# Optimization experiments

Hardware: AMD Instinct MI355X
Metric: run time of the kernel (lower is better)

## Reference

```python
import jax, jax.numpy as jnp
import numpy as np

D_MODEL, D_CTX, D_HEAD = 1024, 768, 16

def setup_inputs() -> dict:
    key = jax.random.key(0)
    ks = jax.random.split(key, 10)
    B, M, N = 8, 4096, 4096
    s = lambda d: 1.0 / np.sqrt(d)
    return {
        "x": jax.random.normal(ks[0], (B, M, D_MODEL), dtype=jnp.float32),
        "context": jax.random.normal(ks[1], (B, N, D_CTX), dtype=jnp.float32),
        "Wq": jax.random.uniform(ks[2], (D_MODEL, D_HEAD), jnp.float32, -s(D_MODEL), s(D_MODEL)),
        "bq": jax.random.uniform(ks[3], (D_HEAD,), jnp.float32, -s(D_MODEL), s(D_MODEL)),
        "Wk": jax.random.uniform(ks[4], (D_CTX, D_HEAD), jnp.float32, -s(D_CTX), s(D_CTX)),
        "bk": jax.random.uniform(ks[5], (D_HEAD,), jnp.float32, -s(D_CTX), s(D_CTX)),
        "Wv": jax.random.uniform(ks[6], (D_CTX, D_HEAD), jnp.float32, -s(D_CTX), s(D_CTX)),
        "bv": jax.random.uniform(ks[7], (D_HEAD,), jnp.float32, -s(D_CTX), s(D_CTX)),
        "Wo": jax.random.uniform(ks[8], (D_HEAD, D_MODEL), jnp.float32, -s(D_HEAD), s(D_HEAD)),
        "bo": jax.random.uniform(ks[9], (D_MODEL,), jnp.float32, -s(D_HEAD), s(D_HEAD)),
    }

def _kernel(t):
    # ELU+1 feature map (non-negative)
    return jax.nn.elu(t) + 1.0

def reference(x, context, Wq, bq, Wk, bk, Wv, bv, Wo, bo):
    Q = _kernel(x @ Wq + bq)            # (B, M, d_head)
    K = _kernel(context @ Wk + bk)      # (B, N, d_head)
    V = context @ Wv + bv               # (B, N, d_head)
    KtV = jnp.einsum('bnd,bne->bde', K, V)   # (B, d_head, d_head)
    num = jnp.einsum('bmd,bde->bme', Q, KtV) # (B, M, d_head)
    K_sum = K.sum(axis=1)                    # (B, d_head)
    denom = jnp.einsum('bmd,bd->bm', Q, K_sum)[..., None] + 1e-6
    out = num / denom                        # (B, M, d_head)
    return out @ Wo + bo                     # (B, M, d_model)
```

## Files before the change

### kernel.cpp

```cpp
#include <hip/hip_runtime.h>
#include <math.h>

#define B_   8
#define M_   4096
#define N_   4096
#define DM   1024
#define DC   768
#define DH   16
#define CHUNKS 64
#define PD   8

typedef float v4f __attribute__((ext_vector_type(4)));
typedef __attribute__((ext_vector_type(8))) short short8v;
typedef __attribute__((ext_vector_type(4))) float f32x4;
typedef __attribute__((ext_vector_type(4))) int int4v;

__device__ __forceinline__ float elu1(float t) {
    return t > 0.0f ? t + 1.0f : expf(t);
}
__device__ __forceinline__ float4 ld4(const float* p) { return *reinterpret_cast<const float4*>(p); }
__device__ __forceinline__ void  st4(float* p, float4 v) { *reinterpret_cast<float4*>(p) = v; }
__device__ __forceinline__ void  st4nt(float* p, float4 v) {
    v4f w; w.x = v.x; w.y = v.y; w.z = v.z; w.w = v.w;
    __builtin_nontemporal_store(w, reinterpret_cast<v4f*>(p));
}
__device__ __forceinline__ void fma4(float4& a, float s, float4 w) {
    a.x = fmaf(s, w.x, a.x); a.y = fmaf(s, w.y, a.y);
    a.z = fmaf(s, w.z, a.z); a.w = fmaf(s, w.w, a.w);
}
__device__ __forceinline__ short f2bf(float f) {
    unsigned u = __float_as_uint(f);
    unsigned r = 0x7FFFu + ((u >> 16) & 1u);
    return (short)((u + r) >> 16);
}
__device__ __forceinline__ unsigned cvtpk(float a, float b) {
    unsigned r;
    asm("v_cvt_pk_bf16_f32 %0, %1, %2" : "=v"(r) : "v"(a), "v"(b));
    return r;
}
__device__ __forceinline__ short8v mk_frag(const float4& a, const float4& b) {
    int4v iv;
    iv.x = (int)cvtpk(a.x, a.y);
    iv.y = (int)cvtpk(a.z, a.w);
    iv.z = (int)cvtpk(b.x, b.y);
    iv.w = (int)cvtpk(b.z, b.w);
    union { int4v i; short8v s; } u; u.i = iv;
    return u.s;
}

__global__ __launch_bounds__(256) void prep(
    const float* __restrict__ Wq, const float* __restrict__ Wk,
    const float* __restrict__ Wv,
    short* __restrict__ fq, short* __restrict__ fk, short* __restrict__ fv)
{
    const int id = blockIdx.x * 256 + threadIdx.x;
    if (id >= 80 * 64) return;
    const int l  = id & 63;
    const int kt = id >> 6;
    const float* W; short* dst; int ktl;
    if (kt < 32)      { W = Wq; dst = fq; ktl = kt; }
    else if (kt < 56) { W = Wk; dst = fk; ktl = kt - 32; }
    else              { W = Wv; dst = fv; ktl = kt - 56; }
    const int k0 = ktl * 32 + (l >> 4) * 8;
    const int d  = l & 15;
    short* o = dst + ((size_t)ktl * 64 + l) * 8;
    #pragma unroll
    for (int j = 0; j < 8; ++j)
        o[j] = f2bf(W[(size_t)(k0 + j) * DH + d]);
}

__global__ __launch_bounds__(256) void fused1(
    const float* __restrict__ ctx, const float* __restrict__ x,
    const short* __restrict__ fq, const short* __restrict__ fk,
    const short* __restrict__ fv,
    const float* __restrict__ bq, const float* __restrict__ bk,
    const float* __restrict__ bv,
    float* __restrict__ part, float* __restrict__ q_ws)
{
    __shared__ float sk[64][DH+1];
    __shared__ float sv[64][DH+1];

    const int t  = threadIdx.x;
    const int l  = t & 63;
    const int w  = t >> 6;
    const int g4 = l >> 4;
    const int lr = l & 15;

    float4 pa[PD], pb[PD];

    if (blockIdx.x < B_*N_/64) {
        const size_t row0 = (size_t)blockIdx.x * 64;
        const float* src = ctx + (row0 + w*16 + lr) * DC + g4*8;
        f32x4 accK = {0,0,0,0}, accV = {0,0,0,0};

        #pragma unroll
        for (int i = 0; i < PD; ++i) {
            pa[i] = ld4(src + i*32);
            pb[i] = ld4(src + i*32 + 4);
        }
        #pragma unroll
        for (int kt = 0; kt < 24; ++kt) {
            const int st = kt & (PD-1);
            const short8v a = mk_frag(pa[st], pb[st]);
            if (kt + PD < 24) {
                pa[st] = ld4(src + (kt+PD)*32);
                pb[st] = ld4(src + (kt+PD)*32 + 4);
            }
            const short8v bkf = *reinterpret_cast<const short8v*>(fk + ((size_t)kt*64 + l)*8);
            const short8v bvf = *reinterpret_cast<const short8v*>(fv + ((size_t)kt*64 + l)*8);
            accK = __builtin_amdgcn_mfma_f32_16x16x32_bf16(a, bkf, accK, 0, 0, 0);
            accV = __builtin_amdgcn_mfma_f32_16x16x32_bf16(a, bvf, accV, 0, 0, 0);
        }

        const float bkv = bk[lr], bvv = bv[lr];
        #pragma unroll
        for (int j = 0; j < 4; ++j) {
            const int n = w*16 + g4*4 + j;
            sk[n][lr] = elu1(accK[j] + bkv);
            sv[n][lr] = accV[j] + bvv;
        }
        __syncthreads();

        const int d = t >> 4, e = t & 15;
        float acc = 0.f;
        #pragma unroll 16
        for (int n = 0; n < 64; ++n) acc += sk[n][d] * sv[n][e];
        float* p = part + (size_t)blockIdx.x * 272;
        p[t] = acc;
        if (t < DH) {
            float ss = 0.f;
            #pragma unroll 16
            for (int n = 0; n < 64; ++n) ss += sk[n][t];
            p[256 + t] = ss;
        }
    } else {
        const size_t row0 = (size_t)(blockIdx.x - B_*N_/64) * 64;
        const float* src = x + (row0 + w*16 + lr) * DM + g4*8;
        f32x4 accQ = {0,0,0,0};

        #pragma unroll
        for (int i = 0; i < PD; ++i) {
            pa[i] = ld4(src + i*32);
            pb[i] = ld4(src + i*32 + 4);
        }
        #pragma unroll
        for (int kt = 0; kt < 32; ++kt) {
            const int st = kt & (PD-1);
            const short8v a = mk_frag(pa[st], pb[st]);
            if (kt + PD < 32) {
                pa[st] = ld4(src + (kt+PD)*32);
                pb[st] = ld4(src + (kt+PD)*32 + 4);
            }
            const short8v bqf = *reinterpret_cast<const short8v*>(fq + ((size_t)kt*64 + l)*8);
            accQ = __builtin_amdgcn_mfma_f32_16x16x32_bf16(a, bqf, accQ, 0, 0, 0);
        }

        const float bqv = bq[lr];
        #pragma unroll
        for (int j = 0; j < 4; ++j) {
            const int n = w*16 + g4*4 + j;
            q_ws[(row0 + n)*DH + lr] = elu1(accQ[j] + bqv);
        }
    }
}

__global__ __launch_bounds__(320) void reduce2(
    const float* __restrict__ part, float* __restrict__ comb)
{
    const int b = blockIdx.x;
    const int t = threadIdx.x;
    if (t < 272) {
        float s = 0.f;
        #pragma unroll
        for (int ch = 0; ch < CHUNKS; ++ch)
            s += part[((size_t)b*CHUNKS + ch) * 272 + t];
        comb[(size_t)b*272 + t] = s;
    }
}

__global__ __launch_bounds__(256) void oproj(
    const float* __restrict__ q_ws, const float* __restrict__ comb,
    const float* __restrict__ Wo, const float* __restrict__ bo,
    float* __restrict__ out)
{
    __shared__ float ql[16 * DH];
    __shared__ float ol[16 * DH];
    __shared__ float kts[272];

    const int t = threadIdx.x;
    const size_t row0 = (size_t)blockIdx.x * 16;
    const int b = blockIdx.x >> 8;

    float4 wreg[16];
    #pragma unroll
    for (int e = 0; e < 16; ++e) wreg[e] = ld4(Wo + (size_t)e*DM + t*4);
    const float4 bov = ld4(bo + t*4);

    if (t < 64) st4(&ql[t*4], ld4(q_ws + row0*DH + t*4));
    else if (t < 132) st4(&kts[(t-64)*4], ld4(comb + (size_t)b*272 + (t-64)*4));
    __syncthreads();

    if (t < 64) {
        const float* qrow = &ql[(t >> 2) * DH];
        const int jj = (t & 3) * 4;
        float den = 1e-6f;
        float4 num = make_float4(0,0,0,0);
        #pragma unroll
        for (int d4 = 0; d4 < 4; ++d4) {
            const float4 q4  = ld4(&qrow[d4*4]);
            const float4 ks4 = ld4(&kts[256 + d4*4]);
            den += q4.x*ks4.x + q4.y*ks4.y + q4.z*ks4.z + q4.w*ks4.w;
            fma4(num, q4.x, ld4(&kts[(d4*4+0)*DH + jj]));
            fma4(num, q4.y, ld4(&kts[(d4*4+1)*DH + jj]));
            fma4(num, q4.z, ld4(&kts[(d4*4+2)*DH + jj]));
            fma4(num, q4.w, ld4(&kts[(d4*4+3)*DH + jj]));
        }
        const float inv = 1.0f / den;
        float4 o4; o4.x = num.x*inv; o4.y = num.y*inv; o4.z = num.z*inv; o4.w = num.w*inv;
        st4(&ol[(t >> 2)*DH + jj], o4);
    }
    __syncthreads();

    #pragma unroll
    for (int r = 0; r < 16; ++r) {
        float4 a = bov;
        #pragma unroll
        for (int eo = 0; eo < 4; ++eo) {
            const float4 o4 = ld4(&ol[r*DH + eo*4]);
            fma4(a, o4.x, wreg[eo*4+0]); fma4(a, o4.y, wreg[eo*4+1]);
            fma4(a, o4.z, wreg[eo*4+2]); fma4(a, o4.w, wreg[eo*4+3]);
        }
        st4nt(out + (row0 + r)*DM + t*4, a);
    }
}

extern "C" void kernel_launch(void* const* d_in, const int* in_sizes, int n_in,
                              void* d_out, int out_size, void* d_ws, size_t ws_size,
                              hipStream_t stream) {
    const float* x    = (const float*)d_in[0];
    const float* ctx  = (const float*)d_in[1];
    const float* Wq   = (const float*)d_in[2];
    const float* bq   = (const float*)d_in[3];
    const float* Wk   = (const float*)d_in[4];
    const float* bk   = (const float*)d_in[5];
    const float* Wv   = (const float*)d_in[6];
    const float* bv   = (const float*)d_in[7];
    const float* Wo   = (const float*)d_in[8];
    const float* bo   = (const float*)d_in[9];
    float* out = (float*)d_out;

    float* ws = (float*)d_ws;
    float* part = ws;
    float* comb = part + (size_t)512*272;
    float* q_ws = comb + (size_t)B_*272;
    short* fq = (short*)(q_ws + (size_t)B_*M_*DH);
    short* fk = fq + (size_t)32*64*8;
    short* fv = fk + (size_t)24*64*8;

    prep<<<dim3(20), dim3(256), 0, stream>>>(Wq, Wk, Wv, fq, fk, fv);
    fused1<<<dim3(B_*N_/64 + B_*M_/64), dim3(256), 0, stream>>>(
        ctx, x, fq, fk, fv, bq, bk, bv, part, q_ws);
    reduce2<<<dim3(B_), dim3(320), 0, stream>>>(part, comb);
    oproj<<<dim3(B_*M_/16), dim3(256), 0, stream>>>(q_ws, comb, Wo, bo, out);
}
```

Baseline: 79.75 us.

## Split projection K dimension across warps with 32-row blocks and LDS reduction

Each block of the fused projection kernel now handles 32 rows instead of 64, with two warps splitting the reduction (K) dimension in half and combining partial MFMA accumulators through shared memory before applying bias and ELU. This doubles the block count and halves the per-warp serial MFMA/load chain, aiming for more memory-level parallelism and better load balance across CUs. It adds an extra LDS round-trip and barrier, and doubles the number of partial KtV slices that reduce2 must sum.

```diff
diff --git a/kernel.cpp b/kernel.cpp
--- a/kernel.cpp
+++ b/kernel.cpp
@@ -7,8 +7,10 @@
 #define DM   1024
 #define DC   768
 #define DH   16
-#define CHUNKS 64
 #define PD   8
+#define KVBLOCKS (B_*N_/32)
+#define QBLOCKS  (B_*M_/32)
+#define CHUNKS   128
 
 typedef float v4f __attribute__((ext_vector_type(4)));
 typedef __attribute__((ext_vector_type(8))) short short8v;
@@ -77,20 +79,31 @@
     const float* __restrict__ bv,
     float* __restrict__ part, float* __restrict__ q_ws)
 {
-    __shared__ float sk[64][DH+1];
-    __shared__ float sv[64][DH+1];
+    __shared__ union {
+        struct {
+            float ka[2][2][16][17];
+            float va[2][2][16][17];
+            float sk[32][17];
+            float sv[32][17];
+        } kv;
+        struct {
+            float qa[2][2][16][17];
+        } q;
+    } sh;
 
     const int t  = threadIdx.x;
     const int l  = t & 63;
     const int w  = t >> 6;
+    const int rt = w & 1;
+    const int kh = w >> 1;
     const int g4 = l >> 4;
     const int lr = l & 15;
 
     float4 pa[PD], pb[PD];
 
-    if (blockIdx.x < B_*N_/64) {
-        const size_t row0 = (size_t)blockIdx.x * 64;
-        const float* src = ctx + (row0 + w*16 + lr) * DC + g4*8;
+    if (blockIdx.x < KVBLOCKS) {
+        const size_t row0 = (size_t)blockIdx.x * 32;
+        const float* src = ctx + (row0 + rt*16 + lr) * DC + kh*384 + g4*8;
         f32x4 accK = {0,0,0,0}, accV = {0,0,0,0};
 
         #pragma unroll
@@ -99,43 +112,53 @@
             pb[i] = ld4(src + i*32 + 4);
         }
         #pragma unroll
-        for (int kt = 0; kt < 24; ++kt) {
+        for (int kt = 0; kt < 12; ++kt) {
             const int st = kt & (PD-1);
             const short8v a = mk_frag(pa[st], pb[st]);
-            if (kt + PD < 24) {
+            if (kt + PD < 12) {
                 pa[st] = ld4(src + (kt+PD)*32);
                 pb[st] = ld4(src + (kt+PD)*32 + 4);
             }
-            const short8v bkf = *reinterpret_cast<const short8v*>(fk + ((size_t)kt*64 + l)*8);
-            const short8v bvf = *reinterpret_cast<const short8v*>(fv + ((size_t)kt*64 + l)*8);
+            const int ktg = kh*12 + kt;
+            const short8v bkf = *reinterpret_cast<const short8v*>(fk + ((size_t)ktg*64 + l)*8);
+            const short8v bvf = *reinterpret_cast<const short8v*>(fv + ((size_t)ktg*64 + l)*8);
             accK = __builtin_amdgcn_mfma_f32_16x16x32_bf16(a, bkf, accK, 0, 0, 0);
             accV = __builtin_amdgcn_mfma_f32_16x16x32_bf16(a, bvf, accV, 0, 0, 0);
         }
 
-        const float bkv = bk[lr], bvv = bv[lr];
         #pragma unroll
         for (int j = 0; j < 4; ++j) {
-            const int n = w*16 + g4*4 + j;
-            sk[n][lr] = elu1(accK[j] + bkv);
-            sv[n][lr] = accV[j] + bvv;
+            sh.kv.ka[rt][kh][g4*4 + j][lr] = accK[j];
+            sh.kv.va[rt][kh][g4*4 + j][lr] = accV[j];
+        }
+        __syncthreads();
+
+        #pragma unroll
+        for (int i = t; i < 512; i += 256) {
+            const int r = i >> 4, c = i & 15;
+            const int rr = r >> 4, wr = r & 15;
+            const float kk = sh.kv.ka[rr][0][wr][c] + sh.kv.ka[rr][1][wr][c] + bk[c];
+            const float vv = sh.kv.va[rr][0][wr][c] + sh.kv.va[rr][1][wr][c] + bv[c];
+            sh.kv.sk[r][c] = elu1(kk);
+            sh.kv.sv[r][c] = vv;
         }
         __syncthreads();
 
         const int d = t >> 4, e = t & 15;
         float acc = 0.f;
         #pragma unroll 16
-        for (int n = 0; n < 64; ++n) acc += sk[n][d] * sv[n][e];
+        for (int n = 0; n < 32; ++n) acc += sh.kv.sk[n][d] * sh.kv.sv[n][e];
         float* p = part + (size_t)blockIdx.x * 272;
         p[t] = acc;
         if (t < DH) {
             float ss = 0.f;
             #pragma unroll 16
-            for (int n = 0; n < 64; ++n) ss += sk[n][t];
+            for (int n = 0; n < 32; ++n) ss += sh.kv.sk[n][t];
             p[256 + t] = ss;
         }
     } else {
-        const size_t row0 = (size_t)(blockIdx.x - B_*N_/64) * 64;
-        const float* src = x + (row0 + w*16 + lr) * DM + g4*8;
+        const size_t row0 = (size_t)(blockIdx.x - KVBLOCKS) * 32;
+        const float* src = x + (row0 + rt*16 + lr) * DM + kh*512 + g4*8;
         f32x4 accQ = {0,0,0,0};
 
         #pragma unroll
@@ -144,22 +167,29 @@
             pb[i] = ld4(src + i*32 + 4);
         }
         #pragma unroll
-        for (int kt = 0; kt < 32; ++kt) {
+        for (int kt = 0; kt < 16; ++kt) {
             const int st = kt & (PD-1);
             const short8v a = mk_frag(pa[st], pb[st]);
-            if (kt + PD < 32) {
+            if (kt + PD < 16) {
                 pa[st] = ld4(src + (kt+PD)*32);
                 pb[st] = ld4(src + (kt+PD)*32 + 4);
             }
-            const short8v bqf = *reinterpret_cast<const short8v*>(fq + ((size_t)kt*64 + l)*8);
+            const int ktg = kh*16 + kt;
+            const short8v bqf = *reinterpret_cast<const short8v*>(fq + ((size_t)ktg*64 + l)*8);
             accQ = __builtin_amdgcn_mfma_f32_16x16x32_bf16(a, bqf, accQ, 0, 0, 0);
         }
 
-        const float bqv = bq[lr];
-        #pragma unroll
-        for (int j = 0; j < 4; ++j) {
-            const int n = w*16 + g4*4 + j;
-            q_ws[(row0 + n)*DH + lr] = elu1(accQ[j] + bqv);
+        #pragma unroll
+        for (int j = 0; j < 4; ++j)
+            sh.q.qa[rt][kh][g4*4 + j][lr] = accQ[j];
+        __syncthreads();
+
+        #pragma unroll
+        for (int i = t; i < 512; i += 256) {
+            const int r = i >> 4, c = i & 15;
+            const int rr = r >> 4, wr = r & 15;
+            const float v = sh.q.qa[rr][0][wr][c] + sh.q.qa[rr][1][wr][c] + bq[c];
+            q_ws[(row0 + r)*DH + c] = elu1(v);
         }
     }
 }
@@ -251,14 +281,14 @@
 
     float* ws = (float*)d_ws;
     float* part = ws;
-    float* comb = part + (size_t)512*272;
+    float* comb = part + (size_t)KVBLOCKS*272;
     float* q_ws = comb + (size_t)B_*272;
     short* fq = (short*)(q_ws + (size_t)B_*M_*DH);
     short* fk = fq + (size_t)32*64*8;
     short* fv = fk + (size_t)24*64*8;
 
     prep<<<dim3(20), dim3(256), 0, stream>>>(Wq, Wk, Wv, fq, fk, fv);
-    fused1<<<dim3(B_*N_/64 + B_*M_/64), dim3(256), 0, stream>>>(
+    fused1<<<dim3(KVBLOCKS + QBLOCKS), dim3(256), 0, stream>>>(
         ctx, x, fq, fk, fv, bq, bk, bv, part, q_ws);
     reduce2<<<dim3(B_), dim3(320), 0, stream>>>(part, comb);
     oproj<<<dim3(B_*M_/16), dim3(256), 0, stream>>>(q_ws, comb, Wo, bo, out);
```

New measurement: 81.29 us. About the same (+1.9%).
